# Optimization experiments

Measured on AMD Instinct MI355X. Metric: run time of the kernel, lower is better.

The kernel has to match this reference:

```python
import jax, jax.numpy as jnp
import numpy as np

EPS_RHO = 1e-8
EPS_DEN = 1e-9


def _rho_signed_sqrt(x):
    return jnp.sqrt(jax.nn.relu(x) + EPS_RHO) - jnp.sqrt(jax.nn.relu(-x) + EPS_RHO)


def setup_inputs() -> dict:
    key = jax.random.key(0)
    ks = jax.random.split(key, 8)
    B, N, C, A = 2, 512, 1024, 64  # batch, seq, hidden_dim, attn_dim
    s_c = 1.0 / np.sqrt(C)
    s_a = 1.0 / np.sqrt(A)
    return {
        "X": jax.random.normal(ks[0], (B, N, C), jnp.float32),
        "Wq": jax.random.normal(ks[1], (A, C), jnp.float32) * s_c,   # Linear(C->A), no bias
        "Wk": jax.random.normal(ks[2], (A, C), jnp.float32) * s_c,   # Linear(C->A), no bias
        "Wphi": jax.random.normal(ks[3], (A,), jnp.float32) * s_a,   # Linear(A->1), no bias
        "Wy_w": jax.random.normal(ks[4], (C, C), jnp.float32) * s_c, # Linear(C->C)
        "Wy_b": jax.random.normal(ks[5], (C,), jnp.float32) * s_c,
        "We_w": jax.random.normal(ks[6], (C, A), jnp.float32) * s_a, # Linear(A->C)
        "We_b": jax.random.normal(ks[7], (C,), jnp.float32) * s_a,
    }


def reference(X, Wq, Wk, Wphi, Wy_w, Wy_b, We_w, We_b):
    # q, k: (B,N,A); Vy: (B,N,C)
    q = jnp.einsum('bnc,ac->bna', X, Wq)
    k = jnp.einsum('bnc,ac->bna', X, Wk)
    Vy = jnp.einsum('bnc,dc->bnd', X, Wy_w) + Wy_b

    # pairwise features e_ij = relu(rho(q_i + k_j)): (B,N,N,A)
    e = jax.nn.relu(_rho_signed_sqrt(q[:, :, None, :] + k[:, None, :, :]))

    # scores: (B,N,N); stable exp with per-row max (== online-softmax result)
    scores = jnp.einsum('bija,a->bij', e, Wphi)
    m = jnp.max(scores, axis=-1, keepdims=True)
    ex = jnp.exp(scores - m)
    denom = jnp.sum(ex, axis=-1)  # (B,N)

    # part1 = exp_scores @ Vy
    part1 = jnp.einsum('bij,bjc->bic', ex, Vy)
    # part2 = sum_j ex_ij * (We e_ij + be) = We(sum_j ex_ij e_ij) + be * denom  (We is linear)
    Ew = jnp.einsum('bij,bija->bia', ex, e)  # (B,N,A)
    part2 = jnp.einsum('bia,ca->bic', Ew, We_w) + We_b * denom[..., None]

    return (part1 + part2) / (denom[..., None] + EPS_DEN)
```

## Files before the change

### kernel.cpp

```cpp
#include <hip/hip_runtime.h>
#include <math.h>

#define EPS_RHO 1e-8f
#define EPS_DEN 1e-9f

constexpr int Bb = 2;
constexpr int Nn = 512;
constexpr int Cc = 1024;
constexpr int Aa = 64;
constexpr int TOK = Bb * Nn;
constexpr int KG  = 640;

typedef __attribute__((ext_vector_type(8))) short short8;
typedef __attribute__((ext_vector_type(4))) float f32x4;

__device__ __forceinline__ float e_fn(float s) {
    const float SQE = 9.9999994e-05f;
    return fmaxf(sqrtf(fmaxf(s, 0.f) + EPS_RHO) - SQE, 0.f);
}

__device__ __forceinline__ short f2bf(float x) {
    union { float f; unsigned u; } v; v.f = x;
    unsigned r = v.u + 0x7FFFu + ((v.u >> 16) & 1u);
    return (short)(r >> 16);
}

__global__ __launch_bounds__(256) void mega_gemm(
    const float* __restrict__ X,
    const float* __restrict__ Wy_w,
    const float* __restrict__ Wq,
    const float* __restrict__ Wk,
    const float* __restrict__ Wy_b,
    short* __restrict__ Gt,
    float* __restrict__ qg,
    float* __restrict__ kg,
    float* __restrict__ kTg)
{
    constexpr int K = 1024, BK = 64;
    __shared__ short As[64][72];
    __shared__ short Bs[64][72];

    int tid = threadIdx.x;
    int bm = blockIdx.y * 64;
    int bn = blockIdx.x * 64;
    int row = tid >> 2;
    int kq  = (tid & 3) << 4;

    const float* ag = X + (size_t)(bm + row) * K + kq;
    int nrow = bn + row;
    const float* bg;
    if (nrow < 1024)      bg = Wy_w + (size_t)nrow * K + kq;
    else if (nrow < 1088) bg = Wq + (size_t)(nrow - 1024) * K + kq;
    else                  bg = Wk + (size_t)(nrow - 1088) * K + kq;

    float4 ar[4], br[4];
    #pragma unroll
    for (int u = 0; u < 4; ++u) {
        ar[u] = *(const float4*)(ag + u * 4);
        br[u] = *(const float4*)(bg + u * 4);
    }

    int wid = tid >> 6, lane = tid & 63;
    int wm = (wid & 1) * 32, wn = (wid >> 1) * 32;
    int fr = lane & 15, fk = (lane >> 4) * 8;

    f32x4 acc[2][2] = {};

    for (int step = 0; step < K / BK; ++step) {
        __syncthreads();
        short tmpA[16], tmpB[16];
        #pragma unroll
        for (int u = 0; u < 4; ++u) {
            tmpA[u*4+0] = f2bf(ar[u].x); tmpA[u*4+1] = f2bf(ar[u].y);
            tmpA[u*4+2] = f2bf(ar[u].z); tmpA[u*4+3] = f2bf(ar[u].w);
            tmpB[u*4+0] = f2bf(br[u].x); tmpB[u*4+1] = f2bf(br[u].y);
            tmpB[u*4+2] = f2bf(br[u].z); tmpB[u*4+3] = f2bf(br[u].w);
        }
        *(short8*)&As[row][kq]     = *(short8*)&tmpA[0];
        *(short8*)&As[row][kq + 8] = *(short8*)&tmpA[8];
        *(short8*)&Bs[row][kq]     = *(short8*)&tmpB[0];
        *(short8*)&Bs[row][kq + 8] = *(short8*)&tmpB[8];
        __syncthreads();

        if (step + 1 < K / BK) {
            const float* ag2 = ag + (size_t)(step + 1) * BK;
            const float* bg2 = bg + (size_t)(step + 1) * BK;
            #pragma unroll
            for (int u = 0; u < 4; ++u) {
                ar[u] = *(const float4*)(ag2 + u * 4);
                br[u] = *(const float4*)(bg2 + u * 4);
            }
        }

        #pragma unroll
        for (int kk = 0; kk < 2; ++kk) {
            short8 af[2], bfr[2];
            #pragma unroll
            for (int mi = 0; mi < 2; ++mi)
                af[mi] = *(const short8*)&As[wm + mi * 16 + fr][kk * 32 + fk];
            #pragma unroll
            for (int ni = 0; ni < 2; ++ni)
                bfr[ni] = *(const short8*)&Bs[wn + ni * 16 + fr][kk * 32 + fk];
            #pragma unroll
            for (int mi = 0; mi < 2; ++mi)
                #pragma unroll
                for (int ni = 0; ni < 2; ++ni)
                    acc[mi][ni] = __builtin_amdgcn_mfma_f32_16x16x32_bf16(
                        af[mi], bfr[ni], acc[mi][ni], 0, 0, 0);
        }
    }

    int cr = (lane >> 4) * 4;
    int cc = lane & 15;
    if (bn < 1024) {
        #pragma unroll
        for (int mi = 0; mi < 2; ++mi)
            #pragma unroll
            for (int ni = 0; ni < 2; ++ni) {
                int c = bn + wn + ni * 16 + cc;
                float bv = Wy_b[c];
                #pragma unroll
                for (int r_ = 0; r_ < 4; ++r_) {
                    int t = bm + wm + mi * 16 + cr + r_;
                    int b = t >> 9, j = t & 511;
                    Gt[((size_t)(b * 1024 + c)) * KG + j] = f2bf(acc[mi][ni][r_] + bv);
                }
            }
    } else if (bn == 1024) {
        #pragma unroll
        for (int mi = 0; mi < 2; ++mi)
            #pragma unroll
            for (int ni = 0; ni < 2; ++ni) {
                int a = wn + ni * 16 + cc;
                #pragma unroll
                for (int r_ = 0; r_ < 4; ++r_) {
                    int t = bm + wm + mi * 16 + cr + r_;
                    qg[(size_t)t * Aa + a] = acc[mi][ni][r_];
                }
            }
    } else {
        #pragma unroll
        for (int mi = 0; mi < 2; ++mi)
            #pragma unroll
            for (int ni = 0; ni < 2; ++ni) {
                int a = wn + ni * 16 + cc;
                #pragma unroll
                for (int r_ = 0; r_ < 4; ++r_) {
                    int t = bm + wm + mi * 16 + cr + r_;
                    int b = t >> 9, j = t & 511;
                    float v = acc[mi][ni][r_];
                    kg[((size_t)(b * 512 + j)) * Aa + a] = v;
                    kTg[((size_t)(b * 64 + a)) * 512 + j] = v;
                }
            }
    }
}

__global__ __launch_bounds__(256) void weprep(
    const float* __restrict__ We_w, short* __restrict__ Gt)
{
    int i = blockIdx.x * 256 + threadIdx.x;
    int s = i & 127;
    int c = (i >> 7) & 1023;
    int b = i >> 17;
    short v = (s < 64) ? f2bf(We_w[(size_t)c * Aa + s]) : (short)0;
    Gt[((size_t)(b * 1024 + c)) * KG + 512 + s] = v;
}

__global__ __launch_bounds__(256) void attn1_kernel(
    const float* __restrict__ qg, const float* __restrict__ kg,
    const float* __restrict__ kTg, const float* __restrict__ Wphi,
    short* __restrict__ P, float* __restrict__ denomg)
{
    __shared__ __align__(16) float qs[Aa];
    __shared__ __align__(16) float wphi[Aa];
    __shared__ __align__(16) float exs[Nn];
    __shared__ __align__(16) float red[256];
    __shared__ __align__(16) float ewp[4][Aa];

    int t = blockIdx.x;
    int b = t >> 9;
    int tid = threadIdx.x;

    if (tid < Aa) {
        qs[tid] = qg[(size_t)t * Aa + tid];
        wphi[tid] = Wphi[tid];
    }
    __syncthreads();

    const float* kT = kTg + (size_t)b * Aa * 512;

    int j0 = tid, j1 = tid + 256;
    float s0 = 0.f, s1 = 0.f;
    #pragma unroll 8
    for (int a = 0; a < Aa; ++a) {
        float qa = qs[a], wa = wphi[a];
        const float* kr = kT + (size_t)a * 512;
        s0 += wa * e_fn(qa + kr[j0]);
        s1 += wa * e_fn(qa + kr[j1]);
    }
    float lmax = fmaxf(s0, s1);

    red[tid] = lmax;
    __syncthreads();
    for (int off = 128; off > 0; off >>= 1) {
        if (tid < off) red[tid] = fmaxf(red[tid], red[tid + off]);
        __syncthreads();
    }
    float m = red[0];
    __syncthreads();

    float e0 = expf(s0 - m), e1 = expf(s1 - m);
    exs[j0] = e0; exs[j1] = e1;
    P[(size_t)t * KG + j0] = f2bf(e0);
    P[(size_t)t * KG + j1] = f2bf(e1);

    red[tid] = e0 + e1;
    __syncthreads();
    for (int off = 128; off > 0; off >>= 1) {
        if (tid < off) red[tid] += red[tid + off];
        __syncthreads();
    }
    if (tid == 0) denomg[t] = red[0];
    __syncthreads();

    {
        int a = tid & 63, grp = tid >> 6;
        const float* kbase = kg + (size_t)b * 512 * Aa;
        float p = 0.f;
        int jb = grp * 128;
        for (int j = jb; j < jb + 128; ++j) {
            float e = e_fn(qs[a] + kbase[(size_t)j * Aa + a]);
            p += exs[j] * e;
        }
        ewp[grp][a] = p;
    }
    __syncthreads();
    if (tid < Aa) {
        float ew = ewp[0][tid] + ewp[1][tid] + ewp[2][tid] + ewp[3][tid];
        P[(size_t)t * KG + 512 + tid] = f2bf(ew);
    } else if (tid < 128) {
        P[(size_t)t * KG + 576 + (tid - 64)] = 0;
    }
}

__global__ __launch_bounds__(256) void attn2_gemm(
    const short* __restrict__ P,
    const short* __restrict__ Gt,
    const float* __restrict__ We_b,
    const float* __restrict__ denomg,
    float* __restrict__ out)
{
    constexpr int BK = 64, NSTEP = KG / BK;
    __shared__ short As[64][72];
    __shared__ short Bs[64][72];

    int tid = threadIdx.x;
    int bm = blockIdx.y * 64, bn = blockIdx.x * 64;
    int b = bm >> 9;
    int row = tid >> 2;
    int kq  = (tid & 3) << 4;

    const short* ap = P  + (size_t)(bm + row) * KG + kq;
    const short* bp = Gt + ((size_t)(b * 1024 + bn + row)) * KG + kq;

    short8 ar[2], br[2];
    ar[0] = *(const short8*)ap;       ar[1] = *(const short8*)(ap + 8);
    br[0] = *(const short8*)bp;       br[1] = *(const short8*)(bp + 8);

    int wid = tid >> 6, lane = tid & 63;
    int wm = (wid & 1) * 32, wn = (wid >> 1) * 32;
    int fr = lane & 15, fk = (lane >> 4) * 8;

    f32x4 acc[2][2] = {};

    for (int step = 0; step < NSTEP; ++step) {
        __syncthreads();
        *(short8*)&As[row][kq]     = ar[0];
        *(short8*)&As[row][kq + 8] = ar[1];
        *(short8*)&Bs[row][kq]     = br[0];
        *(short8*)&Bs[row][kq + 8] = br[1];
        __syncthreads();

        if (step + 1 < NSTEP) {
            const short* ap2 = ap + (size_t)(step + 1) * BK;
            const short* bp2 = bp + (size_t)(step + 1) * BK;
            ar[0] = *(const short8*)ap2;  ar[1] = *(const short8*)(ap2 + 8);
            br[0] = *(const short8*)bp2;  br[1] = *(const short8*)(bp2 + 8);
        }

        #pragma unroll
        for (int kk = 0; kk < 2; ++kk) {
            short8 af[2], bfr[2];
            #pragma unroll
            for (int mi = 0; mi < 2; ++mi)
                af[mi] = *(const short8*)&As[wm + mi * 16 + fr][kk * 32 + fk];
            #pragma unroll
            for (int ni = 0; ni < 2; ++ni)
                bfr[ni] = *(const short8*)&Bs[wn + ni * 16 + fr][kk * 32 + fk];
            #pragma unroll
            for (int mi = 0; mi < 2; ++mi)
                #pragma unroll
                for (int ni = 0; ni < 2; ++ni)
                    acc[mi][ni] = __builtin_amdgcn_mfma_f32_16x16x32_bf16(
                        af[mi], bfr[ni], acc[mi][ni], 0, 0, 0);
        }
    }

    int cr = (lane >> 4) * 4;
    int cc = lane & 15;
    #pragma unroll
    for (int mi = 0; mi < 2; ++mi)
        #pragma unroll
        for (int ni = 0; ni < 2; ++ni) {
            int c = bn + wn + ni * 16 + cc;
            float bv = We_b[c];
            #pragma unroll
            for (int r_ = 0; r_ < 4; ++r_) {
                int t = bm + wm + mi * 16 + cr + r_;
                float dn = denomg[t];
                out[(size_t)t * Cc + c] = (acc[mi][ni][r_] + bv * dn) / (dn + EPS_DEN);
            }
        }
}

extern "C" void kernel_launch(void* const* d_in, const int* in_sizes, int n_in,
                              void* d_out, int out_size, void* d_ws, size_t ws_size,
                              hipStream_t stream)
{
    const float* X    = (const float*)d_in[0];
    const float* Wq   = (const float*)d_in[1];
    const float* Wk   = (const float*)d_in[2];
    const float* Wphi = (const float*)d_in[3];
    const float* Wy_w = (const float*)d_in[4];
    const float* Wy_b = (const float*)d_in[5];
    const float* We_w = (const float*)d_in[6];
    const float* We_b = (const float*)d_in[7];
    float* out = (float*)d_out;

    float* ws = (float*)d_ws;
    float* qg     = ws;
    float* kg     = qg + (size_t)TOK * Aa;
    float* kTg    = kg + (size_t)TOK * Aa;
    float* denomg = kTg + (size_t)TOK * Aa;
    short* Gt     = (short*)(denomg + 1024);
    short* P      = Gt + (size_t)2 * 1024 * KG;

    weprep<<<1024, 256, 0, stream>>>(We_w, Gt);

    dim3 gg(18, 16);
    mega_gemm<<<gg, 256, 0, stream>>>(X, Wy_w, Wq, Wk, Wy_b, Gt, qg, kg, kTg);

    attn1_kernel<<<TOK, 256, 0, stream>>>(qg, kg, kTg, Wphi, P, denomg);

    dim3 g2(16, 16);
    attn2_gemm<<<g2, 256, 0, stream>>>(P, Gt, We_b, denomg, out);
}
```

Before: 140.7 us.

## Reuse score-pass features for weighted sum and drop the softmax max pass

The attention kernel now packs each pairwise feature to bf16 in shared memory during the score pass. It reuses those values for the exp-weighted feature sum instead of recomputing sqrt features from a separate row-major k copy, which also removes the k buffer and its writes from the projection GEMM. The per-row max reduction is removed and exp is applied to raw scores, saving a block reduction and several barriers. This relies on scores staying small enough to avoid overflow, and it lowers the precision of the feature sum by using bf16 features.

```diff
diff --git a/kernel.cpp b/kernel.cpp
--- a/kernel.cpp
+++ b/kernel.cpp
@@ -16,13 +16,19 @@
 
 __device__ __forceinline__ float e_fn(float s) {
     const float SQE = 9.9999994e-05f;
-    return fmaxf(sqrtf(fmaxf(s, 0.f) + EPS_RHO) - SQE, 0.f);
+    return sqrtf(fmaxf(s, 0.f) + EPS_RHO) - SQE;
 }
 
 __device__ __forceinline__ short f2bf(float x) {
     union { float f; unsigned u; } v; v.f = x;
     unsigned r = v.u + 0x7FFFu + ((v.u >> 16) & 1u);
     return (short)(r >> 16);
+}
+
+__device__ __forceinline__ unsigned cvt_pk_bf16(float e0, float e1) {
+    unsigned d;
+    asm("v_cvt_pk_bf16_f32 %0, %1, %2" : "=v"(d) : "v"(e0), "v"(e1));
+    return d;
 }
 
 __global__ __launch_bounds__(256) void mega_gemm(
@@ -33,7 +39,6 @@
     const float* __restrict__ Wy_b,
     short* __restrict__ Gt,
     float* __restrict__ qg,
-    float* __restrict__ kg,
     float* __restrict__ kTg)
 {
     constexpr int K = 1024, BK = 64;
@@ -148,9 +153,7 @@
                 for (int r_ = 0; r_ < 4; ++r_) {
                     int t = bm + wm + mi * 16 + cr + r_;
                     int b = t >> 9, j = t & 511;
-                    float v = acc[mi][ni][r_];
-                    kg[((size_t)(b * 512 + j)) * Aa + a] = v;
-                    kTg[((size_t)(b * 64 + a)) * 512 + j] = v;
+                    kTg[((size_t)(b * 64 + a)) * 512 + j] = acc[mi][ni][r_];
                 }
             }
     }
@@ -167,14 +170,17 @@
     Gt[((size_t)(b * 1024 + c)) * KG + 512 + s] = v;
 }
 
-__global__ __launch_bounds__(256) void attn1_kernel(
-    const float* __restrict__ qg, const float* __restrict__ kg,
-    const float* __restrict__ kTg, const float* __restrict__ Wphi,
-    short* __restrict__ P, float* __restrict__ denomg)
+__global__ __launch_bounds__(256) void attn1_fused(
+    const float* __restrict__ qg,
+    const float* __restrict__ kTg,
+    const float* __restrict__ Wphi,
+    short* __restrict__ P,
+    float* __restrict__ denomg)
 {
     __shared__ __align__(16) float qs[Aa];
-    __shared__ __align__(16) float wphi[Aa];
-    __shared__ __align__(16) float exs[Nn];
+    __shared__ __align__(16) float wph[Aa];
+    __shared__ __align__(16) short E[256][72];
+    __shared__ __align__(16) float exs[256];
     __shared__ __align__(16) float red[256];
     __shared__ __align__(16) float ewp[4][Aa];
 
@@ -184,57 +190,63 @@
 
     if (tid < Aa) {
         qs[tid] = qg[(size_t)t * Aa + tid];
-        wphi[tid] = Wphi[tid];
+        wph[tid] = Wphi[tid];
     }
     __syncthreads();
 
     const float* kT = kTg + (size_t)b * Aa * 512;
 
-    int j0 = tid, j1 = tid + 256;
-    float s0 = 0.f, s1 = 0.f;
-    #pragma unroll 8
-    for (int a = 0; a < Aa; ++a) {
-        float qa = qs[a], wa = wphi[a];
-        const float* kr = kT + (size_t)a * 512;
-        s0 += wa * e_fn(qa + kr[j0]);
-        s1 += wa * e_fn(qa + kr[j1]);
-    }
-    float lmax = fmaxf(s0, s1);
-
-    red[tid] = lmax;
-    __syncthreads();
-    for (int off = 128; off > 0; off >>= 1) {
-        if (tid < off) red[tid] = fmaxf(red[tid], red[tid + off]);
-        __syncthreads();
-    }
-    float m = red[0];
-    __syncthreads();
-
-    float e0 = expf(s0 - m), e1 = expf(s1 - m);
-    exs[j0] = e0; exs[j1] = e1;
-    P[(size_t)t * KG + j0] = f2bf(e0);
-    P[(size_t)t * KG + j1] = f2bf(e1);
-
-    red[tid] = e0 + e1;
+    float dsum = 0.f;
+    float ewacc = 0.f;
+    int pa = tid & 63;
+    int pg = tid >> 6;
+
+    #pragma unroll
+    for (int c = 0; c < 2; ++c) {
+        int j = c * 256 + tid;
+
+        float s = 0.f;
+        #pragma unroll
+        for (int a0 = 0; a0 < Aa; a0 += 8) {
+            float e[8];
+            #pragma unroll
+            for (int u = 0; u < 8; ++u) {
+                float kv = kT[(size_t)(a0 + u) * 512 + j];
+                e[u] = e_fn(qs[a0 + u] + kv);
+                s += wph[a0 + u] * e[u];
+            }
+            uint4 pk;
+            pk.x = cvt_pk_bf16(e[0], e[1]);
+            pk.y = cvt_pk_bf16(e[2], e[3]);
+            pk.z = cvt_pk_bf16(e[4], e[5]);
+            pk.w = cvt_pk_bf16(e[6], e[7]);
+            *(uint4*)&E[tid][a0] = pk;
+        }
+        float ex = expf(s);
+        exs[tid] = ex;
+        dsum += ex;
+        P[(size_t)t * KG + j] = f2bf(ex);
+        __syncthreads();
+
+        #pragma unroll 8
+        for (int jj = 0; jj < 64; ++jj) {
+            int jr = pg * 64 + jj;
+            unsigned ue = (unsigned)(unsigned short)E[jr][pa];
+            float ev = __uint_as_float(ue << 16);
+            ewacc += exs[jr] * ev;
+        }
+        __syncthreads();
+    }
+
+    red[tid] = dsum;
     __syncthreads();
     for (int off = 128; off > 0; off >>= 1) {
         if (tid < off) red[tid] += red[tid + off];
         __syncthreads();
     }
     if (tid == 0) denomg[t] = red[0];
-    __syncthreads();
-
-    {
-        int a = tid & 63, grp = tid >> 6;
-        const float* kbase = kg + (size_t)b * 512 * Aa;
-        float p = 0.f;
-        int jb = grp * 128;
-        for (int j = jb; j < jb + 128; ++j) {
-            float e = e_fn(qs[a] + kbase[(size_t)j * Aa + a]);
-            p += exs[j] * e;
-        }
-        ewp[grp][a] = p;
-    }
+
+    ewp[pg][pa] = ewacc;
     __syncthreads();
     if (tid < Aa) {
         float ew = ewp[0][tid] + ewp[1][tid] + ewp[2][tid] + ewp[3][tid];
@@ -340,8 +352,7 @@
 
     float* ws = (float*)d_ws;
     float* qg     = ws;
-    float* kg     = qg + (size_t)TOK * Aa;
-    float* kTg    = kg + (size_t)TOK * Aa;
+    float* kTg    = qg + (size_t)TOK * Aa;
     float* denomg = kTg + (size_t)TOK * Aa;
     short* Gt     = (short*)(denomg + 1024);
     short* P      = Gt + (size_t)2 * 1024 * KG;
@@ -349,9 +360,9 @@
     weprep<<<1024, 256, 0, stream>>>(We_w, Gt);
 
     dim3 gg(18, 16);
-    mega_gemm<<<gg, 256, 0, stream>>>(X, Wy_w, Wq, Wk, Wy_b, Gt, qg, kg, kTg);
-
-    attn1_kernel<<<TOK, 256, 0, stream>>>(qg, kg, kTg, Wphi, P, denomg);
+    mega_gemm<<<gg, 256, 0, stream>>>(X, Wy_w, Wq, Wk, Wy_b, Gt, qg, kTg);
+
+    attn1_fused<<<TOK, 256, 0, stream>>>(qg, kTg, Wphi, P, denomg);
 
     dim3 g2(16, 16);
     attn2_gemm<<<g2, 256, 0, stream>>>(P, Gt, We_b, denomg, out);
```

New measurement: 122.8 us. 1.15x faster.
